# Optimization experiments

Hardware: AMD Instinct MI355X
Metric: run time of the kernel (lower is better)

The kernel has to match this reference:

```python
import jax, jax.numpy as jnp
import numpy as np

IN_F, OUT_F, GS = 4096, 4096, 128
N_GROUPS = OUT_F * IN_F // GS  # 131072
TOKENS = 8192  # batch 4 * seq 2048


def setup_inputs() -> dict:
    key = jax.random.key(0)
    k1, k2, k3 = jax.random.split(key, 3)
    x = jax.random.normal(k1, (TOKENS, IN_F), dtype=jnp.float32)
    # ternary values in {-1, 0, 1}
    ternary = jax.random.randint(k2, (OUT_F, IN_F), -1, 2, dtype=jnp.int32).astype(jnp.int8)
    # per-group positive scales (beta), like abs-mean init, clamped > 0
    scales = jax.random.uniform(k3, (N_GROUPS,), dtype=jnp.float32, minval=0.01, maxval=0.1)
    ste_gain = jnp.ones((1,), dtype=jnp.float32)
    ste_temp = jnp.ones((1,), dtype=jnp.float32)
    return {"x": x, "ternary": ternary, "scales": scales,
            "ste_gain": ste_gain, "ste_temp": ste_temp}


def reference(x, ternary, scales, ste_gain, ste_temp):
    # Dequantize: each group of GS consecutive weights (row-major over [out,in])
    # shares one scale. scale_exp has shape [OUT_F, IN_F].
    scale_exp = jnp.repeat(scales, GS).reshape(OUT_F, IN_F)
    w = ternary.astype(jnp.float32) * scale_exp  # [out, in]
    # F.linear(x, w) = x @ w.T  (ste_gain/ste_temp affect only backward)
    return jnp.dot(x, w.T)
```

## Files before the change

### kernel.cpp

```cpp
#include <hip/hip_runtime.h>

#define TOKENS 8192
#define IN_F   4096
#define OUT_F  4096

#define BM 256
#define BN 256
#define BK 64
#define NT (IN_F / BK)

typedef __attribute__((ext_vector_type(4))) float  f32x4;
typedef __attribute__((ext_vector_type(4))) int    i32x4;

typedef const __attribute__((address_space(1))) void gas_void;
typedef __attribute__((address_space(3))) void las_void;

__global__ __launch_bounds__(256) void quant_x_kernel(const float* __restrict__ x,
                                                      signed char* __restrict__ xq,
                                                      float* __restrict__ dx) {
    const int row  = blockIdx.x;
    const int tid  = threadIdx.x;
    const int lane = tid & 63;
    const int wv   = tid >> 6;
    const float* xr = x + (size_t)row * IN_F;

    float v[16];
#pragma unroll
    for (int k = 0; k < 4; ++k) {
        f32x4 t = *(const f32x4*)(xr + k * 1024 + tid * 4);
#pragma unroll
        for (int j = 0; j < 4; ++j) v[k * 4 + j] = t[j];
    }
    float m = 0.f;
#pragma unroll
    for (int j = 0; j < 16; ++j) m = fmaxf(m, fabsf(v[j]));
#pragma unroll
    for (int off = 32; off >= 1; off >>= 1) m = fmaxf(m, __shfl_xor(m, off));
    __shared__ float sm[4];
    if (lane == 0) sm[wv] = m;
    __syncthreads();
    m = fmaxf(fmaxf(sm[0], sm[1]), fmaxf(sm[2], sm[3]));

    const float inv = 127.0f / m;
    if (tid == 0) dx[row] = m * (1.0f / 127.0f);

    int* out = (int*)(xq + (size_t)row * IN_F);
#pragma unroll
    for (int k = 0; k < 4; ++k) {
        int p = 0;
#pragma unroll
        for (int j = 0; j < 4; ++j) {
            int q = (int)rintf(v[k * 4 + j] * inv);
            p |= (q & 0xff) << (8 * j);
        }
        out[k * 256 + tid] = p;
    }
}

__global__ __launch_bounds__(256) void quant_w_kernel(const int* __restrict__ tern,
                                                      const float* __restrict__ scales,
                                                      signed char* __restrict__ wq,
                                                      float* __restrict__ dw) {
    const int o   = blockIdx.x;
    const int tid = threadIdx.x;
    const float* sr = scales + o * 32;

    float smax = 0.f;
#pragma unroll
    for (int g = 0; g < 32; ++g) smax = fmaxf(smax, sr[g]);
    if (tid == 0) dw[o] = smax * (1.0f / 127.0f);

    const int g  = tid >> 3;
    const int iq = (int)rintf(sr[g] * (127.0f / smax));

    const i32x4* tp = (const i32x4*)(tern + (size_t)o * IN_F + tid * 16);
    i32x4 out;
#pragma unroll
    for (int k = 0; k < 4; ++k) {
        i32x4 t = tp[k];
        int p = 0;
#pragma unroll
        for (int j = 0; j < 4; ++j) p |= ((t[j] * iq) & 0xff) << (8 * j);
        out[k] = p;
    }
    *(i32x4*)(wq + (size_t)o * IN_F + tid * 16) = out;
}


#define QUAD(MI0, NI0)                                                         \
  do {                                                                         \
    __builtin_amdgcn_s_setprio(1);                                             \
    _Pragma("unroll") for (int mi = 0; mi < 4; ++mi)                           \
      _Pragma("unroll") for (int ni = 0; ni < 2; ++ni)                         \
          acc[(MI0)+mi][(NI0)+ni] = __builtin_amdgcn_mfma_i32_16x16x64_i8(     \
              a[(MI0)+mi], b[(NI0)+ni], acc[(MI0)+mi][(NI0)+ni], 0, 0, 0);     \
    __builtin_amdgcn_s_setprio(0);                                             \
  } while (0)

__global__ __launch_bounds__(512, 2) void gemm_i8_kernel(
        const signed char* __restrict__ A,
        const signed char* __restrict__ B,
        const float* __restrict__ dX,
        const float* __restrict__ dW,
        float* __restrict__ C) {
    __shared__ __align__(16) signed char As[3 * 16384];
    __shared__ __align__(16) signed char Bs[3 * 16384];

    const int tid  = threadIdx.x;
    const int wave = tid >> 6;
    const int lane = tid & 63;
    const int wm   = wave >> 2;
    const int wn   = wave & 3;
    const int lg   = lane >> 4;
    const int lr   = lane & 15;

    int bid = blockIdx.x;
    bid = (bid & 7) * (512 >> 3) + (bid >> 3);
    const int bm = bid >> 4;
    const int bn = bid & 15;

    const size_t a_row0 = (size_t)bm * BM;
    const size_t b_row0 = (size_t)bn * BN;

    const int sx  = (tid & 7) ^ ((tid >> 3) & 7);
    const int s_r = ((tid >> 3) << 1) | ((sx >> 2) & 1);
    const int s_c = (sx & 3) << 4;

    auto stage_unit = [&](int buf, int which, int k0) {
        const int h = which & 1;
        const signed char* G = (which < 2) ? A : B;
        const size_t grow0 = ((which < 2) ? a_row0 : b_row0) + (size_t)h * 128;
        signed char* dstb = ((which < 2) ? As : Bs) + buf * 16384 + h * 8192;
        const signed char* src = G + (grow0 + s_r) * IN_F + k0 + s_c;
        __builtin_amdgcn_global_load_lds((gas_void*)src,
                                         (las_void*)(dstb + (wave << 10)), 16, 0, 0);
    };

    i32x4 acc[8][4] = {};
    i32x4 a[8], b[4];

    auto physoff = [&](int r, int c0) {
        return ((r >> 1) << 7) + (((((r & 1) << 6) | c0) ^ (((r >> 1) & 7) << 4)));
    };
    int pA[8], pB[4];
#pragma unroll
    for (int mi = 0; mi < 8; ++mi) pA[mi] = physoff(wm * 128 + mi * 16 + lr, lg << 4);
#pragma unroll
    for (int ni = 0; ni < 4; ++ni) pB[ni] = physoff(wn * 64 + ni * 16 + lr, lg << 4);

    stage_unit(0, 0, 0); stage_unit(0, 1, 0); stage_unit(0, 2, 0); stage_unit(0, 3, 0);
    stage_unit(1, 0, BK); stage_unit(1, 1, BK); stage_unit(1, 2, BK); stage_unit(1, 3, BK);

    int cur = 0;
    for (int t = 0; t < NT; ++t) {
        if (t + 1 < NT) {
            asm volatile("s_waitcnt vmcnt(4)" ::: "memory");
        } else {
            asm volatile("s_waitcnt vmcnt(0)" ::: "memory");
        }
        __builtin_amdgcn_sched_barrier(0);
        __builtin_amdgcn_s_barrier();
        __builtin_amdgcn_sched_barrier(0);

        const int abase = cur * 16384;
        int s2 = cur + 2; if (s2 >= 3) s2 -= 3;

#pragma unroll
        for (int mi = 0; mi < 8; ++mi) a[mi] = *(const i32x4*)&As[abase + pA[mi]];
#pragma unroll
        for (int ni = 0; ni < 4; ++ni) b[ni] = *(const i32x4*)&Bs[abase + pB[ni]];

        if (t + 2 < NT) {
            const int k2 = (t + 2) * BK;
            stage_unit(s2, 0, k2); stage_unit(s2, 1, k2);
            stage_unit(s2, 2, k2); stage_unit(s2, 3, k2);
        }

        QUAD(0, 0); QUAD(0, 2); QUAD(4, 0); QUAD(4, 2);

        cur = (cur == 2) ? 0 : cur + 1;
    }

    float dwc[4];
#pragma unroll
    for (int ni = 0; ni < 4; ++ni) dwc[ni] = dW[b_row0 + wn * 64 + ni * 16 + lr];

    float* Cp = C + (a_row0 + wm * 128) * (size_t)OUT_F + b_row0 + wn * 64;
#pragma unroll
    for (int mi = 0; mi < 8; ++mi) {
#pragma unroll
        for (int j = 0; j < 4; ++j) {
            const int r = mi * 16 + lg * 4 + j;
            const float dxr = dX[a_row0 + wm * 128 + r];
#pragma unroll
            for (int ni = 0; ni < 4; ++ni)
                Cp[(size_t)r * OUT_F + ni * 16 + lr] =
                    (float)acc[mi][ni][j] * dxr * dwc[ni];
        }
    }
}

extern "C" void kernel_launch(void* const* d_in, const int* in_sizes, int n_in,
                              void* d_out, int out_size, void* d_ws, size_t ws_size,
                              hipStream_t stream) {
    const float* x      = (const float*)d_in[0];
    const int*   tern   = (const int*)d_in[1];
    const float* scales = (const float*)d_in[2];

    signed char* xq = (signed char*)d_ws;
    signed char* wq = xq + (size_t)TOKENS * IN_F;
    float*       dx = (float*)(wq + (size_t)OUT_F * IN_F);
    float*       dw = dx + TOKENS;

    quant_x_kernel<<<TOKENS, 256, 0, stream>>>(x, xq, dx);
    quant_w_kernel<<<OUT_F, 256, 0, stream>>>(tern, scales, wq, dw);

    dim3 grid((TOKENS / BM) * (OUT_F / BN));
    gemm_i8_kernel<<<grid, 512, 0, stream>>>(xq, wq, dx, dw, (float*)d_out);
}
```

Baseline: 179.8 us.

## Load B fragments directly from global into registers, drop B LDS staging

The weight operand B no longer goes through LDS. Each wave loads its B fragments straight from global memory into double-buffered registers one k-step ahead. Only A is staged through the triple-buffered LDS, which halves LDS use and the LDS read traffic, and the loop is unrolled by two with adjusted vmcnt waits. The cost is that the four waves sharing a B column now fetch it redundantly from global/L2, and direct register loads may have exposed latency.

```diff
diff --git a/kernel.cpp b/kernel.cpp
--- a/kernel.cpp
+++ b/kernel.cpp
@@ -87,14 +87,33 @@
 }
 
 
-#define QUAD(MI0, NI0)                                                         \
+#define QUAD(MI0, NI0, BC)                                                     \
   do {                                                                         \
     __builtin_amdgcn_s_setprio(1);                                             \
     _Pragma("unroll") for (int mi = 0; mi < 4; ++mi)                           \
       _Pragma("unroll") for (int ni = 0; ni < 2; ++ni)                         \
           acc[(MI0)+mi][(NI0)+ni] = __builtin_amdgcn_mfma_i32_16x16x64_i8(     \
-              a[(MI0)+mi], b[(NI0)+ni], acc[(MI0)+mi][(NI0)+ni], 0, 0, 0);     \
+              a[(MI0)+mi], BC[(NI0)+ni], acc[(MI0)+mi][(NI0)+ni], 0, 0, 0);    \
     __builtin_amdgcn_s_setprio(0);                                             \
+  } while (0)
+
+#define BODY(T, BC, BNX)                                                       \
+  do {                                                                         \
+    const int c_    = (T) % 3;                                                 \
+    const int abase = c_ * 16384;                                              \
+    _Pragma("unroll") for (int mi = 0; mi < 8; ++mi)                           \
+        a[mi] = *(const i32x4*)&As[abase + pA[mi]];                            \
+    if ((T) + 1 < NT) {                                                        \
+      _Pragma("unroll") for (int ni = 0; ni < 4; ++ni)                         \
+          BNX[ni] = *(const i32x4*)(bp[ni] + ((T) + 1) * BK);                  \
+    }                                                                          \
+    if ((T) + 2 < NT) stage_tile(((T) + 2) % 3, ((T) + 2) * BK);               \
+    QUAD(0, 0, BC); QUAD(0, 2, BC); QUAD(4, 0, BC); QUAD(4, 2, BC);            \
+    if ((T) + 2 < NT)      asm volatile("s_waitcnt vmcnt(6)" ::: "memory");    \
+    else if ((T) + 1 < NT) asm volatile("s_waitcnt vmcnt(4)" ::: "memory");    \
+    __builtin_amdgcn_sched_barrier(0);                                         \
+    __builtin_amdgcn_s_barrier();                                              \
+    __builtin_amdgcn_sched_barrier(0);                                         \
   } while (0)
 
 __global__ __launch_bounds__(512, 2) void gemm_i8_kernel(
@@ -104,7 +123,6 @@
         const float* __restrict__ dW,
         float* __restrict__ C) {
     __shared__ __align__(16) signed char As[3 * 16384];
-    __shared__ __align__(16) signed char Bs[3 * 16384];
 
     const int tid  = threadIdx.x;
     const int wave = tid >> 6;
@@ -126,59 +144,39 @@
     const int s_r = ((tid >> 3) << 1) | ((sx >> 2) & 1);
     const int s_c = (sx & 3) << 4;
 
-    auto stage_unit = [&](int buf, int which, int k0) {
-        const int h = which & 1;
-        const signed char* G = (which < 2) ? A : B;
-        const size_t grow0 = ((which < 2) ? a_row0 : b_row0) + (size_t)h * 128;
-        signed char* dstb = ((which < 2) ? As : Bs) + buf * 16384 + h * 8192;
-        const signed char* src = G + (grow0 + s_r) * IN_F + k0 + s_c;
-        __builtin_amdgcn_global_load_lds((gas_void*)src,
-                                         (las_void*)(dstb + (wave << 10)), 16, 0, 0);
+    auto stage_half = [&](int buf, int h, int k0) {
+        const signed char* src = A + (a_row0 + h * 128 + s_r) * IN_F + k0 + s_c;
+        signed char* dst = As + buf * 16384 + h * 8192 + (wave << 10);
+        __builtin_amdgcn_global_load_lds((gas_void*)src, (las_void*)dst, 16, 0, 0);
     };
+    auto stage_tile = [&](int buf, int k0) { stage_half(buf, 0, k0); stage_half(buf, 1, k0); };
 
     i32x4 acc[8][4] = {};
-    i32x4 a[8], b[4];
+    i32x4 a[8], bA[4], bB[4];
 
     auto physoff = [&](int r, int c0) {
         return ((r >> 1) << 7) + (((((r & 1) << 6) | c0) ^ (((r >> 1) & 7) << 4)));
     };
-    int pA[8], pB[4];
+    int pA[8];
 #pragma unroll
     for (int mi = 0; mi < 8; ++mi) pA[mi] = physoff(wm * 128 + mi * 16 + lr, lg << 4);
-#pragma unroll
-    for (int ni = 0; ni < 4; ++ni) pB[ni] = physoff(wn * 64 + ni * 16 + lr, lg << 4);
-
-    stage_unit(0, 0, 0); stage_unit(0, 1, 0); stage_unit(0, 2, 0); stage_unit(0, 3, 0);
-    stage_unit(1, 0, BK); stage_unit(1, 1, BK); stage_unit(1, 2, BK); stage_unit(1, 3, BK);
-
-    int cur = 0;
-    for (int t = 0; t < NT; ++t) {
-        if (t + 1 < NT) {
-            asm volatile("s_waitcnt vmcnt(4)" ::: "memory");
-        } else {
-            asm volatile("s_waitcnt vmcnt(0)" ::: "memory");
-        }
-        __builtin_amdgcn_sched_barrier(0);
-        __builtin_amdgcn_s_barrier();
-        __builtin_amdgcn_sched_barrier(0);
-
-        const int abase = cur * 16384;
-        int s2 = cur + 2; if (s2 >= 3) s2 -= 3;
-
-#pragma unroll
-        for (int mi = 0; mi < 8; ++mi) a[mi] = *(const i32x4*)&As[abase + pA[mi]];
-#pragma unroll
-        for (int ni = 0; ni < 4; ++ni) b[ni] = *(const i32x4*)&Bs[abase + pB[ni]];
-
-        if (t + 2 < NT) {
-            const int k2 = (t + 2) * BK;
-            stage_unit(s2, 0, k2); stage_unit(s2, 1, k2);
-            stage_unit(s2, 2, k2); stage_unit(s2, 3, k2);
-        }
-
-        QUAD(0, 0); QUAD(0, 2); QUAD(4, 0); QUAD(4, 2);
-
-        cur = (cur == 2) ? 0 : cur + 1;
+
+    const signed char* bp[4];
+#pragma unroll
+    for (int ni = 0; ni < 4; ++ni)
+        bp[ni] = B + (size_t)(b_row0 + wn * 64 + ni * 16 + lr) * IN_F + lg * 16;
+
+    stage_tile(0, 0); stage_tile(1, BK);
+#pragma unroll
+    for (int ni = 0; ni < 4; ++ni) bA[ni] = *(const i32x4*)(bp[ni] + 0);
+    asm volatile("s_waitcnt vmcnt(0)" ::: "memory");
+    __builtin_amdgcn_sched_barrier(0);
+    __builtin_amdgcn_s_barrier();
+    __builtin_amdgcn_sched_barrier(0);
+
+    for (int tt = 0; tt < NT; tt += 2) {
+        BODY(tt,     bA, bB);
+        BODY(tt + 1, bB, bA);
     }
 
     float dwc[4];
```

Measured after the change: 259.2 us. +44.2%, slower.

## Shrink GEMM tile to 256x128 with 4 waves and XCD-aware block mapping

Applied to the files above, without the earlier changes.

Halves the block tile along N (256x128) and the block to 4 waves, each wave keeping a 128x64 sub-tile. Staging is reworked so each thread issues two async global-to-LDS loads per unit, and B uses a smaller LDS buffer. Blocks are remapped so each XCD owns a contiguous strip of N tiles, which is meant to improve L2 reuse of weight tiles. The grid doubles and LDS per block shrinks, trading more A re-reads for better occupancy and finer load balance.

```diff
diff --git a/kernel.cpp b/kernel.cpp
--- a/kernel.cpp
+++ b/kernel.cpp
@@ -5,7 +5,7 @@
 #define OUT_F  4096
 
 #define BM 256
-#define BN 256
+#define BN 128
 #define BK 64
 #define NT (IN_F / BK)
 
@@ -97,43 +97,55 @@
     __builtin_amdgcn_s_setprio(0);                                             \
   } while (0)
 
-__global__ __launch_bounds__(512, 2) void gemm_i8_kernel(
+__global__ __launch_bounds__(256, 2) void gemm_i8_kernel(
         const signed char* __restrict__ A,
         const signed char* __restrict__ B,
         const float* __restrict__ dX,
         const float* __restrict__ dW,
         float* __restrict__ C) {
     __shared__ __align__(16) signed char As[3 * 16384];
-    __shared__ __align__(16) signed char Bs[3 * 16384];
+    __shared__ __align__(16) signed char Bs[3 * 8192];
 
     const int tid  = threadIdx.x;
     const int wave = tid >> 6;
     const int lane = tid & 63;
-    const int wm   = wave >> 2;
-    const int wn   = wave & 3;
+    const int wm   = wave >> 1;
+    const int wn   = wave & 1;
     const int lg   = lane >> 4;
     const int lr   = lane & 15;
 
-    int bid = blockIdx.x;
-    bid = (bid & 7) * (512 >> 3) + (bid >> 3);
-    const int bm = bid >> 4;
-    const int bn = bid & 15;
+    const int bid    = blockIdx.x;
+    const int xcd    = bid & 7;
+    const int within = bid >> 3;
+    const int bn     = xcd * 4 + (within & 3);
+    const int bm     = within >> 2;
 
     const size_t a_row0 = (size_t)bm * BM;
     const size_t b_row0 = (size_t)bn * BN;
 
-    const int sx  = (tid & 7) ^ ((tid >> 3) & 7);
-    const int s_r = ((tid >> 3) << 1) | ((sx >> 2) & 1);
-    const int s_c = (sx & 3) << 4;
+    int s_r[2], s_c[2];
+#pragma unroll
+    for (int i = 0; i < 2; ++i) {
+        const int u  = i * 256 + tid;
+        const int sx = (u & 7) ^ ((u >> 3) & 7);
+        s_r[i] = ((u >> 3) << 1) | ((sx >> 2) & 1);
+        s_c[i] = (sx & 3) << 4;
+    }
 
     auto stage_unit = [&](int buf, int which, int k0) {
-        const int h = which & 1;
         const signed char* G = (which < 2) ? A : B;
-        const size_t grow0 = ((which < 2) ? a_row0 : b_row0) + (size_t)h * 128;
-        signed char* dstb = ((which < 2) ? As : Bs) + buf * 16384 + h * 8192;
-        const signed char* src = G + (grow0 + s_r) * IN_F + k0 + s_c;
-        __builtin_amdgcn_global_load_lds((gas_void*)src,
-                                         (las_void*)(dstb + (wave << 10)), 16, 0, 0);
+        const size_t grow0 = (which < 2) ? (a_row0 + (size_t)(which & 1) * 128) : b_row0;
+        signed char* dstb = (which < 2) ? (As + buf * 16384 + (which & 1) * 8192)
+                                        : (Bs + buf * 8192);
+#pragma unroll
+        for (int i = 0; i < 2; ++i) {
+            const signed char* src = G + (grow0 + s_r[i]) * IN_F + k0 + s_c[i];
+            signed char* dst = dstb + i * 4096 + (wave << 10);
+            __builtin_amdgcn_global_load_lds((gas_void*)src, (las_void*)dst, 16, 0, 0);
+        }
+    };
+    auto stage_tile = [&](int buf, int k0) {
+        stage_unit(buf, 0, k0); stage_unit(buf, 1, k0); stage_unit(buf, 2, k0);
     };
 
     i32x4 acc[8][4] = {};
@@ -148,13 +160,13 @@
 #pragma unroll
     for (int ni = 0; ni < 4; ++ni) pB[ni] = physoff(wn * 64 + ni * 16 + lr, lg << 4);
 
-    stage_unit(0, 0, 0); stage_unit(0, 1, 0); stage_unit(0, 2, 0); stage_unit(0, 3, 0);
-    stage_unit(1, 0, BK); stage_unit(1, 1, BK); stage_unit(1, 2, BK); stage_unit(1, 3, BK);
+    stage_tile(0, 0);
+    stage_tile(1, BK);
 
     int cur = 0;
     for (int t = 0; t < NT; ++t) {
         if (t + 1 < NT) {
-            asm volatile("s_waitcnt vmcnt(4)" ::: "memory");
+            asm volatile("s_waitcnt vmcnt(6)" ::: "memory");
         } else {
             asm volatile("s_waitcnt vmcnt(0)" ::: "memory");
         }
@@ -163,18 +175,15 @@
         __builtin_amdgcn_sched_barrier(0);
 
         const int abase = cur * 16384;
+        const int bbase = cur * 8192;
         int s2 = cur + 2; if (s2 >= 3) s2 -= 3;
 
 #pragma unroll
         for (int mi = 0; mi < 8; ++mi) a[mi] = *(const i32x4*)&As[abase + pA[mi]];
 #pragma unroll
-        for (int ni = 0; ni < 4; ++ni) b[ni] = *(const i32x4*)&Bs[abase + pB[ni]];
-
-        if (t + 2 < NT) {
-            const int k2 = (t + 2) * BK;
-            stage_unit(s2, 0, k2); stage_unit(s2, 1, k2);
-            stage_unit(s2, 2, k2); stage_unit(s2, 3, k2);
-        }
+        for (int ni = 0; ni < 4; ++ni) b[ni] = *(const i32x4*)&Bs[bbase + pB[ni]];
+
+        if (t + 2 < NT) stage_tile(s2, (t + 2) * BK);
 
         QUAD(0, 0); QUAD(0, 2); QUAD(4, 0); QUAD(4, 2);
 
@@ -216,5 +225,5 @@
     quant_w_kernel<<<OUT_F, 256, 0, stream>>>(tern, scales, wq, dw);
 
     dim3 grid((TOKENS / BM) * (OUT_F / BN));
-    gemm_i8_kernel<<<grid, 512, 0, stream>>>(xq, wq, dx, dw, (float*)d_out);
-}
+    gemm_i8_kernel<<<grid, 256, 0, stream>>>(xq, wq, dx, dw, (float*)d_out);
+}
```

Result: slower. 189.9 us (+5.6%).

## Replace block barrier with LDS flag-based producer/consumer sync and 4-stage ring

Applied to the files above, without the earlier changes.

Replaces the per-iteration workgroup s_barrier with per-buffer LDS counters that waves atomically increment and spin on. Waves 0-3 now load only A and waves 4-7 only B, and the ring grows from 3 to 4 stages. The aim is to let waves drift out of lockstep so barrier stalls stop serialising MFMA and load issue. The cost is higher LDS use (128KB+), which with launch bounds of 2 blocks per CU may cut occupancy, plus spin-wait overhead and LDS atomics.

```diff
diff --git a/kernel.cpp b/kernel.cpp
--- a/kernel.cpp
+++ b/kernel.cpp
@@ -93,8 +93,14 @@
     _Pragma("unroll") for (int mi = 0; mi < 4; ++mi)                           \
       _Pragma("unroll") for (int ni = 0; ni < 2; ++ni)                         \
           acc[(MI0)+mi][(NI0)+ni] = __builtin_amdgcn_mfma_i32_16x16x64_i8(     \
-              a[(MI0)+mi], b[(NI0)+ni], acc[(MI0)+mi][(NI0)+ni], 0, 0, 0);     \
+              a[(MI0)+mi], bf[(NI0)+ni], acc[(MI0)+mi][(NI0)+ni], 0, 0, 0);    \
     __builtin_amdgcn_s_setprio(0);                                             \
+  } while (0)
+
+#define SPIN_GE(IDX, TGT)                                                      \
+  do {                                                                         \
+    while (*(volatile int*)&flg[IDX] < (TGT)) __builtin_amdgcn_s_sleep(2);     \
+    __builtin_amdgcn_sched_barrier(0);                                         \
   } while (0)
 
 __global__ __launch_bounds__(512, 2) void gemm_i8_kernel(
@@ -103,8 +109,9 @@
         const float* __restrict__ dX,
         const float* __restrict__ dW,
         float* __restrict__ C) {
-    __shared__ __align__(16) signed char As[3 * 16384];
-    __shared__ __align__(16) signed char Bs[3 * 16384];
+    __shared__ __align__(16) signed char As[4 * 16384];
+    __shared__ __align__(16) signed char Bs[4 * 16384];
+    __shared__ int flg[8];
 
     const int tid  = threadIdx.x;
     const int wave = tid >> 6;
@@ -122,22 +129,35 @@
     const size_t a_row0 = (size_t)bm * BM;
     const size_t b_row0 = (size_t)bn * BN;
 
-    const int sx  = (tid & 7) ^ ((tid >> 3) & 7);
-    const int s_r = ((tid >> 3) << 1) | ((sx >> 2) & 1);
-    const int s_c = (sx & 3) << 4;
-
-    auto stage_unit = [&](int buf, int which, int k0) {
-        const int h = which & 1;
-        const signed char* G = (which < 2) ? A : B;
-        const size_t grow0 = ((which < 2) ? a_row0 : b_row0) + (size_t)h * 128;
-        signed char* dstb = ((which < 2) ? As : Bs) + buf * 16384 + h * 8192;
-        const signed char* src = G + (grow0 + s_r) * IN_F + k0 + s_c;
-        __builtin_amdgcn_global_load_lds((gas_void*)src,
-                                         (las_void*)(dstb + (wave << 10)), 16, 0, 0);
+    if (tid < 8) flg[tid] = 0;
+    __syncthreads();
+
+    const bool wavA = (wave < 4);
+    const signed char* gbase[4];
+    int dstoff[4];
+#pragma unroll
+    for (int i = 0; i < 4; ++i) {
+        const int j  = wave * 4 + i;
+        const int u  = (j & 7) * 64 + lane;
+        const int sx = (u & 7) ^ ((u >> 3) & 7);
+        const int srow = ((u >> 3) << 1) | ((sx >> 2) & 1);
+        const int scol = (sx & 3) << 4;
+        const size_t grow = (wavA ? a_row0 : b_row0) + (size_t)(((j >> 3) & 1) * 128 + srow);
+        gbase[i]  = (wavA ? A : B) + grow * IN_F + scol;
+        dstoff[i] = ((j >> 3) & 1) * 8192 + (j & 7) * 1024 + lane * 16;
+    }
+    signed char* Ldst = wavA ? As : Bs;
+
+    auto stage = [&](int buf, int k0) {
+#pragma unroll
+        for (int i = 0; i < 4; ++i)
+            __builtin_amdgcn_global_load_lds((gas_void*)(gbase[i] + k0),
+                                             (las_void*)(Ldst + buf * 16384 + dstoff[i]),
+                                             16, 0, 0);
     };
 
     i32x4 acc[8][4] = {};
-    i32x4 a[8], b[4];
+    i32x4 a[8], bf[4];
 
     auto physoff = [&](int r, int c0) {
         return ((r >> 1) << 7) + (((((r & 1) << 6) | c0) ^ (((r >> 1) & 7) << 4)));
@@ -148,37 +168,38 @@
 #pragma unroll
     for (int ni = 0; ni < 4; ++ni) pB[ni] = physoff(wn * 64 + ni * 16 + lr, lg << 4);
 
-    stage_unit(0, 0, 0); stage_unit(0, 1, 0); stage_unit(0, 2, 0); stage_unit(0, 3, 0);
-    stage_unit(1, 0, BK); stage_unit(1, 1, BK); stage_unit(1, 2, BK); stage_unit(1, 3, BK);
-
-    int cur = 0;
+    stage(0, 0);
+    stage(1, BK);
+    asm volatile("s_waitcnt vmcnt(4)" ::: "memory");
+    __builtin_amdgcn_sched_barrier(0);
+    if (lane == 0) atomicAdd(&flg[0], 1);
+
     for (int t = 0; t < NT; ++t) {
-        if (t + 1 < NT) {
+        const int b = t & 3;
+
+        SPIN_GE(b, 8 * (t >> 2) + 8);
+
+#pragma unroll
+        for (int mi = 0; mi < 8; ++mi) a[mi] = *(const i32x4*)&As[b * 16384 + pA[mi]];
+#pragma unroll
+        for (int ni = 0; ni < 4; ++ni) bf[ni] = *(const i32x4*)&Bs[b * 16384 + pB[ni]];
+        QUAD(0, 0); QUAD(0, 2); QUAD(4, 0); QUAD(4, 2);
+
+        __builtin_amdgcn_sched_barrier(0);
+        if (lane == 0) atomicAdd(&flg[4 + b], 1);
+
+        if (t + 2 < NT) {
+            const int s = t + 2, bs = s & 3;
+            SPIN_GE(4 + bs, 8 * (s >> 2));
+            stage(bs, s * BK);
             asm volatile("s_waitcnt vmcnt(4)" ::: "memory");
-        } else {
+            __builtin_amdgcn_sched_barrier(0);
+            if (lane == 0) atomicAdd(&flg[(t + 1) & 3], 1);
+        } else if (t + 1 < NT) {
             asm volatile("s_waitcnt vmcnt(0)" ::: "memory");
+            __builtin_amdgcn_sched_barrier(0);
+            if (lane == 0) atomicAdd(&flg[(t + 1) & 3], 1);
         }
-        __builtin_amdgcn_sched_barrier(0);
-        __builtin_amdgcn_s_barrier();
-        __builtin_amdgcn_sched_barrier(0);
-
-        const int abase = cur * 16384;
-        int s2 = cur + 2; if (s2 >= 3) s2 -= 3;
-
-#pragma unroll
-        for (int mi = 0; mi < 8; ++mi) a[mi] = *(const i32x4*)&As[abase + pA[mi]];
-#pragma unroll
-        for (int ni = 0; ni < 4; ++ni) b[ni] = *(const i32x4*)&Bs[abase + pB[ni]];
-
-        if (t + 2 < NT) {
-            const int k2 = (t + 2) * BK;
-            stage_unit(s2, 0, k2); stage_unit(s2, 1, k2);
-            stage_unit(s2, 2, k2); stage_unit(s2, 3, k2);
-        }
-
-        QUAD(0, 0); QUAD(0, 2); QUAD(4, 0); QUAD(4, 2);
-
-        cur = (cur == 2) ? 0 : cur + 1;
     }
 
     float dwc[4];
```

Measured after the change: 227.1 us. +26.3%, slower.
